# Kernel optimization log

Hardware: AMD Instinct MI355X
Metric: run time of the kernel (lower is better)

## Reference

```python
import math
import jax, jax.numpy as jnp
import numpy as np

PROB_SPARSE_FACTOR = 0.4


def setup_inputs() -> dict:
    key = jax.random.key(0)
    kq, kk, kv = jax.random.split(key, 3)
    B, H, T, S, D = 2, 16, 2048, 2048, 64
    q = jax.random.normal(kq, (B, H, T, D), dtype=jnp.float32)
    k = jax.random.normal(kk, (B, H, S, D), dtype=jnp.float32)
    v = jax.random.normal(kv, (B, H, S, D), dtype=jnp.float32)
    return {"q": q, "k": k, "v": v}


def reference(q, k, v):
    B, H, T, D = q.shape
    S = k.shape[2]
    scaling = 1.0 / math.sqrt(D)
    # Informer-style top-u query count (static, derived from shapes)
    u = max(int(min(PROB_SPARSE_FACTOR * math.log(S), T * 0.5)), int(T * 0.3))

    # KLD scoring over full attention approximation: [B,H,T,S]
    attn_approx = jnp.einsum("bhtd,bhsd->bhts", q * scaling, k)
    attn_approx = jnp.clip(attn_approx, -50.0, 50.0)
    attn_approx = attn_approx - jnp.max(attn_approx, axis=-1, keepdims=True)
    sm = jax.nn.softmax(attn_approx, axis=-1)
    log_uniform = math.log(S)
    kl_score = jnp.sum(sm * (jnp.log(sm + 1e-10) + log_uniform), axis=-1)  # [B,H,T]

    # Select top-u most informative queries per (b,h)
    _, topk_idx = jax.lax.top_k(kl_score, u)  # [B,H,u]

    # Sparse attention only for selected queries
    q_red = jnp.take_along_axis(q, topk_idx[..., None], axis=2)  # [B,H,u,D]
    scores = jnp.einsum("bhud,bhsd->bhus", q_red, k) * scaling
    scores = jnp.clip(scores, -50.0, 50.0)
    scores = scores - jnp.max(scores, axis=-1, keepdims=True)
    w = jax.nn.softmax(scores, axis=-1)
    w = jnp.clip(w, 1e-9, 1.0)
    out_red = jnp.einsum("bhus,bhsd->bhud", w, v)  # [B,H,u,D]

    # Scatter reduced outputs back into a zero-initialized full output
    b_i = jnp.arange(B)[:, None, None]
    h_i = jnp.arange(H)[None, :, None]
    out = jnp.zeros_like(q).at[b_i, h_i, topk_idx].set(out_red)
    return out
```

## Files before the change

### kernel.cpp

```cpp
#include <hip/hip_runtime.h>
#include <math.h>

#define T_DIM 2048
#define S_DIM 2048
#define D_DIM 64
#define BH_DIM 32
#define U_SEL 614
#define QROWS 32
#define LOG_S_D 7.624618986159398
#define LOG2E_F 1.4426950408889634f
#define LN2_D 0.6931471805599453
#define SCL_Q (0.125f * LOG2E_F)

typedef __attribute__((ext_vector_type(8))) short bf16x8;
typedef __attribute__((ext_vector_type(4))) short bf16x4;
typedef __attribute__((ext_vector_type(4))) float f32x4;

__device__ __forceinline__ unsigned short bf16_rne(float x) {
  unsigned u = __float_as_uint(x);
  u += 0x7FFF + ((u >> 16) & 1);
  return (unsigned short)(u >> 16);
}
__device__ __forceinline__ float bf16_to_f(unsigned short h) {
  return __uint_as_float(((unsigned)h) << 16);
}
#if defined(__has_builtin)
#if __has_builtin(__builtin_amdgcn_exp2f)
#define EXP2_HW(x) __builtin_amdgcn_exp2f(x)
#endif
#endif
#ifndef EXP2_HW
#define EXP2_HW(x) exp2f(x)
#endif

#define GLD_LDS16(g, l)                                                        \
  __builtin_amdgcn_global_load_lds(                                            \
      (const __attribute__((address_space(1))) unsigned int*)(const void*)(g), \
      (__attribute__((address_space(3))) unsigned int*)(void*)(l), 16, 0, 0)

__device__ __forceinline__ void stage_img16(const unsigned short* __restrict__ g,
                                            unsigned short* l, int lane, int w) {
#pragma unroll
  for (int it = 0; it < 4; ++it) {
    const int chunk = it * 4 + w;
    GLD_LDS16((const char*)g + chunk * 1024 + lane * 16, (char*)l + chunk * 1024);
  }
}

__device__ __forceinline__ bf16x8 ldfrag_sw(const unsigned short* buf, int row, int chunk) {
  return *(const bf16x8*)(buf + (row << 6) + (((chunk) ^ (row & 7)) << 3));
}

__global__ __launch_bounds__(256) void convert_kernel(
    const float* __restrict__ kin, const float* __restrict__ vin,
    const float* __restrict__ qin, unsigned short* __restrict__ kimg,
    unsigned short* __restrict__ vt_g, unsigned short* __restrict__ qimg,
    unsigned short* __restrict__ kcimg, float* __restrict__ out) {
  __shared__ float vld[128][65];
  const int jb = blockIdx.x;
  const int tid = threadIdx.x;
  if (jb < 2048) {
    const bool isq = jb >= 1024;
    const int jj = jb & 1023;
    const int bh = jj >> 5, tl = jj & 31;
    const float* src = (isq ? qin : kin) + ((size_t)bh * 2048 + tl * 64) * 64;
    unsigned short* dst = (isq ? qimg : kimg) + (size_t)(bh * 32 + tl) * 8192;
    unsigned short* kcd = kcimg + (size_t)(bh * 16 + (tl >> 1)) * 8192;
    const float scl = isq ? SCL_Q : 1.0f;
#pragma unroll
    for (int g = 0; g < 2; ++g) {
      const int flat = g * 256 + tid;
      const int r = flat >> 3, c = flat & 7;
      const float4 f0 = *(const float4*)(src + r * 64 + c * 8);
      const float4 f1 = *(const float4*)(src + r * 64 + c * 8 + 4);
      const float xs[8] = {f0.x, f0.y, f0.z, f0.w, f1.x, f1.y, f1.z, f1.w};
      bf16x8 hv, lv;
#pragma unroll
      for (int j = 0; j < 8; ++j) {
        const float x = xs[j] * scl;
        const unsigned short h = bf16_rne(x);
        hv[j] = (short)h;
        lv[j] = (short)bf16_rne(x - bf16_to_f(h));
      }
      const int base = (r << 6) + ((c ^ (r & 7)) << 3);
      *(bf16x8*)(dst + base) = hv;
      *(bf16x8*)(dst + 4096 + base) = lv;
      if (!isq) {
        const int s_local = ((tl & 1) << 6) + r;
        const int wv = s_local >> 5, mtk = (r >> 4) & 1, kcc = c >> 2, qdd = c & 3;
        *(bf16x8*)(kcd + (wv * 4 + mtk * 2 + kcc) * 512 + qdd * 128 + ((r & 15) << 3)) = hv;
      }
    }
  } else if (jb < 2560) {
    const int jv = jb - 2048;
    const int bh = jv >> 4, tl = jv & 15;
    const float* src = vin + ((size_t)bh * 2048 + tl * 128) * 64;
#pragma unroll
    for (int g = 0; g < 8; ++g) {
      const int f = g * 256 + tid;
      const int r = f >> 4, c4 = f & 15;
      const float4 x = *(const float4*)(src + r * 64 + c4 * 4);
      vld[r][c4 * 4 + 0] = x.x;
      vld[r][c4 * 4 + 1] = x.y;
      vld[r][c4 * 4 + 2] = x.z;
      vld[r][c4 * 4 + 3] = x.w;
    }
    __syncthreads();
    unsigned short* dst = vt_g + (size_t)(bh * 16 + tl) * 8192;
#pragma unroll
    for (int g = 0; g < 4; ++g) {
      const int oc = g * 256 + tid;
      const int w4 = oc >> 8, dt = (oc >> 6) & 3, qd = (oc >> 4) & 3, l = oc & 15;
      bf16x8 hv;
#pragma unroll
      for (int j = 0; j < 8; ++j)
        hv[j] = (short)bf16_rne(vld[w4 * 32 + qd * 8 + j][dt * 16 + l]);
      *(bf16x8*)(dst + oc * 8) = hv;
    }
  } else {
    float4* o4 = (float4*)out;
    const size_t b = (size_t)(jb - 2560);
#pragma unroll
    for (int g = 0; g < 8; ++g)
      o4[b * 2048 + g * 256 + tid] = make_float4(0.f, 0.f, 0.f, 0.f);
  }
}

__global__ __launch_bounds__(256, 2) void kl_score_mfma(
    const unsigned short* __restrict__ qimg, const unsigned short* __restrict__ kimg,
    float2* __restrict__ zw) {
  __shared__ __align__(16) unsigned short lbuf[2][8192];
  const int b = blockIdx.x;
  const int bh = b & 31;
  const int tt = (b >> 5) & 15;
  const int shalf = b >> 9;
  const int tid = threadIdx.x;
  const int lane = tid & 63, w = tid >> 6, quad = lane >> 4, l15 = lane & 15;
  const unsigned short* qb = qimg + (size_t)(bh * 32 + tt * 2) * 8192;
  const unsigned short* kb = kimg + (size_t)bh * (32 * 8192);
  const int tg0 = shalf * 16;

  stage_img16(qb, &lbuf[0][0], lane, w);
  stage_img16(qb + 8192, &lbuf[1][0], lane, w);
  __syncthreads();

  bf16x8 ah[2][2], al[2][2];
#pragma unroll
  for (int rt = 0; rt < 2; ++rt) {
    const int row = w * 32 + rt * 16 + l15;
    const unsigned short* lb = &lbuf[row >> 6][0];
    const int r64 = row & 63;
#pragma unroll
    for (int kc = 0; kc < 2; ++kc) {
      const int off = (r64 << 6) + (((kc * 4 + quad) ^ (r64 & 7)) << 3);
      ah[rt][kc] = *(const bf16x8*)(lb + off);
      al[rt][kc] = *(const bf16x8*)(lb + 4096 + off);
    }
  }
  __syncthreads();

  stage_img16(kb + (size_t)tg0 * 8192, &lbuf[0][0], lane, w);
  __syncthreads();

  float Zf[8], Wf[8];
#pragma unroll
  for (int i = 0; i < 8; ++i) { Zf[i] = 0.f; Wf[i] = 0.f; }

  for (int t = 0; t < 16; ++t) {
    if (t < 15)
      stage_img16(kb + (size_t)(tg0 + t + 1) * 8192, &lbuf[(t + 1) & 1][0], lane, w);
    const unsigned short* cb = &lbuf[t & 1][0];

    f32x4 acc[2][4];
#pragma unroll
    for (int rt = 0; rt < 2; ++rt)
#pragma unroll
      for (int ct = 0; ct < 4; ++ct) acc[rt][ct] = (f32x4){0.f, 0.f, 0.f, 0.f};

#pragma unroll
    for (int ct = 0; ct < 4; ++ct) {
      const int srow = ct * 16 + l15;
      const bf16x8 bh0 = ldfrag_sw(cb, srow, quad);
      const bf16x8 bl0 = ldfrag_sw(cb + 4096, srow, quad);
      const bf16x8 bh1 = ldfrag_sw(cb, srow, 4 + quad);
      const bf16x8 bl1 = ldfrag_sw(cb + 4096, srow, 4 + quad);
#pragma unroll
      for (int rt = 0; rt < 2; ++rt) {
        f32x4 c = acc[rt][ct];
        c = __builtin_amdgcn_mfma_f32_16x16x32_bf16(ah[rt][0], bh0, c, 0, 0, 0);
        c = __builtin_amdgcn_mfma_f32_16x16x32_bf16(al[rt][0], bh0, c, 0, 0, 0);
        c = __builtin_amdgcn_mfma_f32_16x16x32_bf16(ah[rt][0], bl0, c, 0, 0, 0);
        c = __builtin_amdgcn_mfma_f32_16x16x32_bf16(ah[rt][1], bh1, c, 0, 0, 0);
        c = __builtin_amdgcn_mfma_f32_16x16x32_bf16(al[rt][1], bh1, c, 0, 0, 0);
        c = __builtin_amdgcn_mfma_f32_16x16x32_bf16(ah[rt][1], bl1, c, 0, 0, 0);
        acc[rt][ct] = c;
      }
    }

#pragma unroll
    for (int rt = 0; rt < 2; ++rt)
#pragma unroll
      for (int r = 0; r < 4; ++r) {
        float zp = 0.f, wp = 0.f;
#pragma unroll
        for (int ct = 0; ct < 4; ++ct) {
          const float tv = acc[rt][ct][r];
          const float e = EXP2_HW(tv);
          zp += e;
          wp = fmaf(e, tv, wp);
        }
        Zf[rt * 4 + r] += zp;
        Wf[rt * 4 + r] += wp;
      }
    __syncthreads();
  }

#pragma unroll
  for (int i = 0; i < 8; ++i) {
    float Zt = Zf[i], Wt = Wf[i];
#pragma unroll
    for (int mask = 1; mask <= 8; mask <<= 1) {
      Zt += __shfl_xor(Zt, mask);
      Wt += __shfl_xor(Wt, mask);
    }
    if (l15 == 0) {
      const int row = tt * 128 + w * 32 + (i >> 2) * 16 + quad * 4 + (i & 3);
      zw[((size_t)shalf * 32 + bh) * 2048 + row] = make_float2(Zt, Wt);
    }
  }
}

__global__ __launch_bounds__(1024) void topk_kernel(const float2* __restrict__ zw,
                                                    int* __restrict__ topk) {
  __shared__ float sv[2048];
  __shared__ int si[2048];
  const int bh = blockIdx.x;
  const int tid = threadIdx.x;
  for (int i = tid; i < 2048; i += 1024) {
    const float2 a = zw[(size_t)bh * 2048 + i];
    const float2 c = zw[(size_t)(32 + bh) * 2048 + i];
    const double Z = (double)a.x + (double)c.x;
    const double W = (double)a.y + (double)c.y;
    sv[i] = (float)(LN2_D * (W / Z) - log(Z) + LOG_S_D);
    si[i] = i;
  }
  __syncthreads();
  for (int kk = 2; kk <= 2048; kk <<= 1) {
    for (int j = kk >> 1; j > 0; j >>= 1) {
      const int p = tid;
      const int i = ((p & ~(j - 1)) << 1) | (p & (j - 1));
      const int pr = i | j;
      const float v1 = sv[i], v2 = sv[pr];
      const int i1 = si[i], i2 = si[pr];
      const bool beforePI = (v2 > v1) || (v2 == v1 && i2 < i1);
      const bool dirDesc = ((i & kk) == 0);
      const bool doSwap = dirDesc ? beforePI : !beforePI;
      if (doSwap) { sv[i] = v2; sv[pr] = v1; si[i] = i2; si[pr] = i1; }
      __syncthreads();
    }
  }
  for (int i = tid; i < U_SEL; i += 1024) topk[bh * U_SEL + i] = si[i];
}

struct __align__(16) SmC {
  union { unsigned short qs[QROWS * 64]; unsigned short ps[4][QROWS * 40]; } c;
  float obuf[QROWS * 64];
  float zred[4][QROWS];
};

__global__ __launch_bounds__(256, 3) void sparse_attn_mfma(
    const float* __restrict__ q, const unsigned short* __restrict__ kcimg,
    const unsigned short* __restrict__ vt_g, const int* __restrict__ topk,
    float* __restrict__ out) {
  __shared__ SmC sm;
  const int b = blockIdx.x;
  const int bh = b & 31;
  const int l0 = (b >> 5) * QROWS;
  const int tid = threadIdx.x;
  const int lane = tid & 63, w = tid >> 6, quad = lane >> 4, l15 = lane & 15;
  const float* qb = q + (size_t)bh * (2048 * 64);
  const char* kcb = (const char*)(kcimg + (size_t)bh * (16 * 8192));
  const char* vtb = (const char*)(vt_g + (size_t)bh * (16 * 8192));
  const int* tkb = topk + bh * U_SEL;

  {
    const int r = tid >> 3, c = tid & 7;
    const int l = l0 + r;
    const int row = (l < U_SEL) ? tkb[l] : tkb[0];
    const float4 f0 = *(const float4*)(qb + (size_t)row * 64 + c * 8);
    const float4 f1 = *(const float4*)(qb + (size_t)row * 64 + c * 8 + 4);
    const float xs[8] = {f0.x, f0.y, f0.z, f0.w, f1.x, f1.y, f1.z, f1.w};
    bf16x8 hv;
#pragma unroll
    for (int j = 0; j < 8; ++j) hv[j] = (short)bf16_rne(xs[j] * SCL_Q);
    *(bf16x8*)&sm.c.qs[(r << 6) + ((c ^ (r & 7)) << 3)] = hv;
  }
  __syncthreads();

  bf16x8 qf[2][2];
#pragma unroll
  for (int nt = 0; nt < 2; ++nt)
#pragma unroll
    for (int kc = 0; kc < 2; ++kc)
      qf[nt][kc] = ldfrag_sw(sm.c.qs, nt * 16 + l15, kc * 4 + quad);
  __syncthreads();

  float zrun[2] = {0.f, 0.f};
  f32x4 oacc[2][4];
#pragma unroll
  for (int a = 0; a < 2; ++a)
#pragma unroll
    for (int b2 = 0; b2 < 4; ++b2) oacc[a][b2] = (f32x4){0.f, 0.f, 0.f, 0.f};

  const int kvbase = (w * 4) << 10;

#define LOADKV(AF, VB, ST)                                                     \
  do {                                                                         \
    const char* kp_ = kcb + (size_t)(ST) * 16384 + kvbase + lane * 16;         \
    const char* vp_ = vtb + (size_t)(ST) * 16384 + kvbase + lane * 16;         \
    (AF)[0][0] = *(const bf16x8*)(kp_);                                        \
    (AF)[0][1] = *(const bf16x8*)(kp_ + 1024);                                 \
    (AF)[1][0] = *(const bf16x8*)(kp_ + 2048);                                 \
    (AF)[1][1] = *(const bf16x8*)(kp_ + 3072);                                 \
    (VB)[0] = *(const bf16x8*)(vp_);                                           \
    (VB)[1] = *(const bf16x8*)(vp_ + 1024);                                    \
    (VB)[2] = *(const bf16x8*)(vp_ + 2048);                                    \
    (VB)[3] = *(const bf16x8*)(vp_ + 3072);                                    \
  } while (0)

#define COMPUTE(AF, VB)                                                        \
  do {                                                                         \
    f32x4 sacc[2][2];                                                          \
    __builtin_amdgcn_s_setprio(1);                                             \
    _Pragma("unroll") for (int mt = 0; mt < 2; ++mt)                           \
        _Pragma("unroll") for (int nt = 0; nt < 2; ++nt) {                     \
      f32x4 c = (f32x4){0.f, 0.f, 0.f, 0.f};                                   \
      c = __builtin_amdgcn_mfma_f32_16x16x32_bf16((AF)[mt][0], qf[nt][0], c, 0, 0, 0); \
      c = __builtin_amdgcn_mfma_f32_16x16x32_bf16((AF)[mt][1], qf[nt][1], c, 0, 0, 0); \
      sacc[mt][nt] = c;                                                        \
    }                                                                          \
    __builtin_amdgcn_s_setprio(0);                                             \
    _Pragma("unroll") for (int nt = 0; nt < 2; ++nt) {                         \
      float zl = 0.f;                                                          \
      _Pragma("unroll") for (int mt = 0; mt < 2; ++mt) {                       \
        bf16x4 pw;                                                             \
        _Pragma("unroll") for (int r = 0; r < 4; ++r) {                        \
          const float p = EXP2_HW(sacc[mt][nt][r]);                            \
          zl += p;                                                             \
          pw[r] = (short)bf16_rne(p);                                          \
        }                                                                      \
        *(bf16x4*)&sm.c.ps[w][(nt * 16 + l15) * 40 + mt * 16 + quad * 4] = pw; \
      }                                                                        \
      zrun[nt] += zl;                                                          \
    }                                                                          \
    __builtin_amdgcn_s_setprio(1);                                             \
    _Pragma("unroll") for (int mtq = 0; mtq < 2; ++mtq) {                      \
      const bf16x8 pa = *(const bf16x8*)&sm.c.ps[w][(mtq * 16 + l15) * 40 + quad * 8]; \
      _Pragma("unroll") for (int dt = 0; dt < 4; ++dt)                         \
        oacc[mtq][dt] = __builtin_amdgcn_mfma_f32_16x16x32_bf16(pa, (VB)[dt], oacc[mtq][dt], 0, 0, 0); \
    }                                                                          \
    __builtin_amdgcn_s_setprio(0);                                             \
  } while (0)

  bf16x8 afA[2][2], vbfA[4], afB[2][2], vbfB[4];
  LOADKV(afA, vbfA, 0);
  for (int st = 0; st < 16; st += 2) {
    LOADKV(afB, vbfB, st + 1);
    COMPUTE(afA, vbfA);
    if (st + 2 < 16) LOADKV(afA, vbfA, st + 2);
    COMPUTE(afB, vbfB);
  }
#undef LOADKV
#undef COMPUTE

#pragma unroll
  for (int nt = 0; nt < 2; ++nt) {
    float z = zrun[nt];
    z += __shfl_xor(z, 16);
    z += __shfl_xor(z, 32);
    if (quad == 0) sm.zred[w][nt * 16 + l15] = z;
  }
  for (int i = tid; i < QROWS * 64; i += 256) sm.obuf[i] = 0.f;
  __syncthreads();
#pragma unroll
  for (int mtq = 0; mtq < 2; ++mtq)
#pragma unroll
    for (int r = 0; r < 4; ++r) {
      const int qr = mtq * 16 + quad * 4 + r;
#pragma unroll
      for (int dt = 0; dt < 4; ++dt)
        atomicAdd(&sm.obuf[qr * 64 + dt * 16 + l15], oacc[mtq][dt][r]);
    }
  __syncthreads();
  {
    if (tid < QROWS * 4) {
      const int qr = tid >> 2, seg = tid & 3;
      const int l = l0 + qr;
      if (l < U_SEL) {
        const float Zt = sm.zred[0][qr] + sm.zred[1][qr] +
                         sm.zred[2][qr] + sm.zred[3][qr];
        const float inv = 1.0f / Zt;
        const int row = tkb[l];
        float* op = &out[((size_t)bh * T_DIM + row) * 64 + seg * 16];
        const float* ob = &sm.obuf[qr * 64 + seg * 16];
#pragma unroll
        for (int j = 0; j < 4; ++j) {
          float4 o;
          o.x = ob[j * 4 + 0] * inv;
          o.y = ob[j * 4 + 1] * inv;
          o.z = ob[j * 4 + 2] * inv;
          o.w = ob[j * 4 + 3] * inv;
          *(float4*)&op[j * 4] = o;
        }
      }
    }
  }
}

extern "C" void kernel_launch(void* const* d_in, const int* in_sizes, int n_in,
                              void* d_out, int out_size, void* d_ws, size_t ws_size,
                              hipStream_t stream) {
  const float* q = (const float*)d_in[0];
  const float* k = (const float*)d_in[1];
  const float* v = (const float*)d_in[2];
  float* out = (float*)d_out;
  char* ws = (char*)d_ws;
  float2* zw = (float2*)ws;
  int* topk = (int*)(ws + 1048576);
  unsigned short* kimg = (unsigned short*)(ws + 1310720);
  unsigned short* vt_g = (unsigned short*)(ws + 18087936);
  unsigned short* qimg = (unsigned short*)(ws + 26476544);
  unsigned short* kcimg = (unsigned short*)(ws + 43253760);

  convert_kernel<<<dim3(3072), dim3(256), 0, stream>>>(k, v, q, kimg, vt_g, qimg, kcimg, out);
  kl_score_mfma<<<dim3(1024), dim3(256), 0, stream>>>(qimg, kimg, zw);
  topk_kernel<<<dim3(BH_DIM), dim3(1024), 0, stream>>>(zw, topk);
  sparse_attn_mfma<<<dim3(768), dim3(256), 0, stream>>>(q, kcimg, vt_g, topk, out);
}
```

Measured before the change: 218.8 us.

## Move V transpose and output zeroing into the top-k kernel launch

The V bf16 transpose and the output zero-fill move out of the convert kernel and into extra blocks of the top-k launch, which previously ran only 32 blocks. That work now fills otherwise idle CUs while the bitonic sort runs, and the convert kernel shrinks to 2048 blocks. The cost is that the aux blocks use 1024 threads with a shared-memory union, and they could compete with the sort blocks.

```diff
diff --git a/kernel.cpp b/kernel.cpp
--- a/kernel.cpp
+++ b/kernel.cpp
@@ -52,77 +52,41 @@
 }
 
 __global__ __launch_bounds__(256) void convert_kernel(
-    const float* __restrict__ kin, const float* __restrict__ vin,
-    const float* __restrict__ qin, unsigned short* __restrict__ kimg,
-    unsigned short* __restrict__ vt_g, unsigned short* __restrict__ qimg,
-    unsigned short* __restrict__ kcimg, float* __restrict__ out) {
-  __shared__ float vld[128][65];
+    const float* __restrict__ kin, const float* __restrict__ qin,
+    unsigned short* __restrict__ kimg, unsigned short* __restrict__ qimg,
+    unsigned short* __restrict__ kcimg) {
   const int jb = blockIdx.x;
   const int tid = threadIdx.x;
-  if (jb < 2048) {
-    const bool isq = jb >= 1024;
-    const int jj = jb & 1023;
-    const int bh = jj >> 5, tl = jj & 31;
-    const float* src = (isq ? qin : kin) + ((size_t)bh * 2048 + tl * 64) * 64;
-    unsigned short* dst = (isq ? qimg : kimg) + (size_t)(bh * 32 + tl) * 8192;
-    unsigned short* kcd = kcimg + (size_t)(bh * 16 + (tl >> 1)) * 8192;
-    const float scl = isq ? SCL_Q : 1.0f;
-#pragma unroll
-    for (int g = 0; g < 2; ++g) {
-      const int flat = g * 256 + tid;
-      const int r = flat >> 3, c = flat & 7;
-      const float4 f0 = *(const float4*)(src + r * 64 + c * 8);
-      const float4 f1 = *(const float4*)(src + r * 64 + c * 8 + 4);
-      const float xs[8] = {f0.x, f0.y, f0.z, f0.w, f1.x, f1.y, f1.z, f1.w};
-      bf16x8 hv, lv;
-#pragma unroll
-      for (int j = 0; j < 8; ++j) {
-        const float x = xs[j] * scl;
-        const unsigned short h = bf16_rne(x);
-        hv[j] = (short)h;
-        lv[j] = (short)bf16_rne(x - bf16_to_f(h));
-      }
-      const int base = (r << 6) + ((c ^ (r & 7)) << 3);
-      *(bf16x8*)(dst + base) = hv;
-      *(bf16x8*)(dst + 4096 + base) = lv;
-      if (!isq) {
-        const int s_local = ((tl & 1) << 6) + r;
-        const int wv = s_local >> 5, mtk = (r >> 4) & 1, kcc = c >> 2, qdd = c & 3;
-        *(bf16x8*)(kcd + (wv * 4 + mtk * 2 + kcc) * 512 + qdd * 128 + ((r & 15) << 3)) = hv;
-      }
-    }
-  } else if (jb < 2560) {
-    const int jv = jb - 2048;
-    const int bh = jv >> 4, tl = jv & 15;
-    const float* src = vin + ((size_t)bh * 2048 + tl * 128) * 64;
-#pragma unroll
-    for (int g = 0; g < 8; ++g) {
-      const int f = g * 256 + tid;
-      const int r = f >> 4, c4 = f & 15;
-      const float4 x = *(const float4*)(src + r * 64 + c4 * 4);
-      vld[r][c4 * 4 + 0] = x.x;
-      vld[r][c4 * 4 + 1] = x.y;
-      vld[r][c4 * 4 + 2] = x.z;
-      vld[r][c4 * 4 + 3] = x.w;
-    }
-    __syncthreads();
-    unsigned short* dst = vt_g + (size_t)(bh * 16 + tl) * 8192;
-#pragma unroll
-    for (int g = 0; g < 4; ++g) {
-      const int oc = g * 256 + tid;
-      const int w4 = oc >> 8, dt = (oc >> 6) & 3, qd = (oc >> 4) & 3, l = oc & 15;
-      bf16x8 hv;
-#pragma unroll
-      for (int j = 0; j < 8; ++j)
-        hv[j] = (short)bf16_rne(vld[w4 * 32 + qd * 8 + j][dt * 16 + l]);
-      *(bf16x8*)(dst + oc * 8) = hv;
-    }
-  } else {
-    float4* o4 = (float4*)out;
-    const size_t b = (size_t)(jb - 2560);
-#pragma unroll
-    for (int g = 0; g < 8; ++g)
-      o4[b * 2048 + g * 256 + tid] = make_float4(0.f, 0.f, 0.f, 0.f);
+  const bool isq = jb >= 1024;
+  const int jj = jb & 1023;
+  const int bh = jj >> 5, tl = jj & 31;
+  const float* src = (isq ? qin : kin) + ((size_t)bh * 2048 + tl * 64) * 64;
+  unsigned short* dst = (isq ? qimg : kimg) + (size_t)(bh * 32 + tl) * 8192;
+  unsigned short* kcd = kcimg + (size_t)(bh * 16 + (tl >> 1)) * 8192;
+  const float scl = isq ? SCL_Q : 1.0f;
+#pragma unroll
+  for (int g = 0; g < 2; ++g) {
+    const int flat = g * 256 + tid;
+    const int r = flat >> 3, c = flat & 7;
+    const float4 f0 = *(const float4*)(src + r * 64 + c * 8);
+    const float4 f1 = *(const float4*)(src + r * 64 + c * 8 + 4);
+    const float xs[8] = {f0.x, f0.y, f0.z, f0.w, f1.x, f1.y, f1.z, f1.w};
+    bf16x8 hv, lv;
+#pragma unroll
+    for (int j = 0; j < 8; ++j) {
+      const float x = xs[j] * scl;
+      const unsigned short h = bf16_rne(x);
+      hv[j] = (short)h;
+      lv[j] = (short)bf16_rne(x - bf16_to_f(h));
+    }
+    const int base = (r << 6) + ((c ^ (r & 7)) << 3);
+    *(bf16x8*)(dst + base) = hv;
+    *(bf16x8*)(dst + 4096 + base) = lv;
+    if (!isq) {
+      const int s_local = ((tl & 1) << 6) + r;
+      const int wv = s_local >> 5, mtk = (r >> 4) & 1, kcc = c >> 2, qdd = c & 3;
+      *(bf16x8*)(kcd + (wv * 4 + mtk * 2 + kcc) * 512 + qdd * 128 + ((r & 15) << 3)) = hv;
+    }
   }
 }
 
@@ -230,36 +194,74 @@
   }
 }
 
-__global__ __launch_bounds__(1024) void topk_kernel(const float2* __restrict__ zw,
-                                                    int* __restrict__ topk) {
-  __shared__ float sv[2048];
-  __shared__ int si[2048];
-  const int bh = blockIdx.x;
+__global__ __launch_bounds__(1024) void topk_aux_kernel(
+    const float2* __restrict__ zw, int* __restrict__ topk,
+    const float* __restrict__ vin, unsigned short* __restrict__ vt_g,
+    float* __restrict__ out) {
+  __shared__ union {
+    struct { float sv[2048]; int si[2048]; } s;
+    float vld[128][65];
+  } u;
+  const int jb = blockIdx.x;
   const int tid = threadIdx.x;
-  for (int i = tid; i < 2048; i += 1024) {
-    const float2 a = zw[(size_t)bh * 2048 + i];
-    const float2 c = zw[(size_t)(32 + bh) * 2048 + i];
-    const double Z = (double)a.x + (double)c.x;
-    const double W = (double)a.y + (double)c.y;
-    sv[i] = (float)(LN2_D * (W / Z) - log(Z) + LOG_S_D);
-    si[i] = i;
-  }
-  __syncthreads();
-  for (int kk = 2; kk <= 2048; kk <<= 1) {
-    for (int j = kk >> 1; j > 0; j >>= 1) {
-      const int p = tid;
-      const int i = ((p & ~(j - 1)) << 1) | (p & (j - 1));
-      const int pr = i | j;
-      const float v1 = sv[i], v2 = sv[pr];
-      const int i1 = si[i], i2 = si[pr];
-      const bool beforePI = (v2 > v1) || (v2 == v1 && i2 < i1);
-      const bool dirDesc = ((i & kk) == 0);
-      const bool doSwap = dirDesc ? beforePI : !beforePI;
-      if (doSwap) { sv[i] = v2; sv[pr] = v1; si[i] = i2; si[pr] = i1; }
-      __syncthreads();
-    }
-  }
-  for (int i = tid; i < U_SEL; i += 1024) topk[bh * U_SEL + i] = si[i];
+  if (jb < 32) {
+    const int bh = jb;
+    for (int i = tid; i < 2048; i += 1024) {
+      const float2 a = zw[(size_t)bh * 2048 + i];
+      const float2 c = zw[(size_t)(32 + bh) * 2048 + i];
+      const double Z = (double)a.x + (double)c.x;
+      const double W = (double)a.y + (double)c.y;
+      u.s.sv[i] = (float)(LN2_D * (W / Z) - log(Z) + LOG_S_D);
+      u.s.si[i] = i;
+    }
+    __syncthreads();
+    for (int kk = 2; kk <= 2048; kk <<= 1) {
+      for (int j = kk >> 1; j > 0; j >>= 1) {
+        const int p = tid;
+        const int i = ((p & ~(j - 1)) << 1) | (p & (j - 1));
+        const int pr = i | j;
+        const float v1 = u.s.sv[i], v2 = u.s.sv[pr];
+        const int i1 = u.s.si[i], i2 = u.s.si[pr];
+        const bool beforePI = (v2 > v1) || (v2 == v1 && i2 < i1);
+        const bool dirDesc = ((i & kk) == 0);
+        const bool doSwap = dirDesc ? beforePI : !beforePI;
+        if (doSwap) { u.s.sv[i] = v2; u.s.sv[pr] = v1; u.s.si[i] = i2; u.s.si[pr] = i1; }
+        __syncthreads();
+      }
+    }
+    for (int i = tid; i < U_SEL; i += 1024) topk[bh * U_SEL + i] = u.s.si[i];
+  } else if (jb < 544) {
+    const int jv = jb - 32;
+    const int bh = jv >> 4, tl = jv & 15;
+    const float* src = vin + ((size_t)bh * 2048 + tl * 128) * 64;
+#pragma unroll
+    for (int g = 0; g < 2; ++g) {
+      const int f = g * 1024 + tid;
+      const int r = f >> 4, c4 = f & 15;
+      const float4 x = *(const float4*)(src + r * 64 + c4 * 4);
+      u.vld[r][c4 * 4 + 0] = x.x;
+      u.vld[r][c4 * 4 + 1] = x.y;
+      u.vld[r][c4 * 4 + 2] = x.z;
+      u.vld[r][c4 * 4 + 3] = x.w;
+    }
+    __syncthreads();
+    unsigned short* dst = vt_g + (size_t)(bh * 16 + tl) * 8192;
+    {
+      const int oc = tid;
+      const int w4 = oc >> 8, dt = (oc >> 6) & 3, qd = (oc >> 4) & 3, l = oc & 15;
+      bf16x8 hv;
+#pragma unroll
+      for (int j = 0; j < 8; ++j)
+        hv[j] = (short)bf16_rne(u.vld[w4 * 32 + qd * 8 + j][dt * 16 + l]);
+      *(bf16x8*)(dst + oc * 8) = hv;
+    }
+  } else {
+    float4* o4 = (float4*)out;
+    const size_t b = (size_t)(jb - 544);
+#pragma unroll
+    for (int g = 0; g < 4; ++g)
+      o4[b * 4096 + g * 1024 + tid] = make_float4(0.f, 0.f, 0.f, 0.f);
+  }
 }
 
 struct __align__(16) SmC {
@@ -432,8 +434,8 @@
   unsigned short* qimg = (unsigned short*)(ws + 26476544);
   unsigned short* kcimg = (unsigned short*)(ws + 43253760);
 
-  convert_kernel<<<dim3(3072), dim3(256), 0, stream>>>(k, v, q, kimg, vt_g, qimg, kcimg, out);
+  convert_kernel<<<dim3(2048), dim3(256), 0, stream>>>(k, q, kimg, qimg, kcimg);
   kl_score_mfma<<<dim3(1024), dim3(256), 0, stream>>>(qimg, kimg, zw);
-  topk_kernel<<<dim3(BH_DIM), dim3(1024), 0, stream>>>(zw, topk);
+  topk_aux_kernel<<<dim3(800), dim3(1024), 0, stream>>>(zw, topk, v, vt_g, out);
   sparse_attn_mfma<<<dim3(768), dim3(256), 0, stream>>>(q, kcimg, vt_g, topk, out);
 }
```

Measured after the change: 221.4 us. Within noise of the previous version (+1.2%).
